# Performance work log

Hardware: AMD Instinct MI355X
Metric: run time of the kernel (lower is better)

The kernel has to match this reference:

```python
import math
import jax, jax.numpy as jnp
import numpy as np

NUM_BINS = 8
TRANS = 8
LEFT, RIGHT = -1.0, 1.0
MIN_W = MIN_H = MIN_D = 1.0e-4


def setup_inputs() -> dict:
    key = jax.random.key(0)
    ks = jax.random.split(key, 8)
    B, D, H, OUT = 524288, 16, 256, TRANS * (3 * NUM_BINS - 1)
    x = jax.random.uniform(ks[0], (B, D), jnp.float32, -0.99, 0.99)
    W0 = jax.random.normal(ks[1], (8, H), jnp.float32) * (1.0 / math.sqrt(8))
    b0 = jnp.zeros((H,), jnp.float32)
    W1 = jax.random.normal(ks[2], (H, H), jnp.float32) * (1.0 / math.sqrt(H))
    b1 = jnp.zeros((H,), jnp.float32)
    Wout = jax.random.normal(ks[3], (H, OUT), jnp.float32) * (0.1 / math.sqrt(H))
    bout = jnp.zeros((OUT,), jnp.float32)
    return {"x": x, "W0": W0, "b0": b0, "W1": W1, "b1": b1, "Wout": Wout, "bout": bout}


def _rq_spline(x, raw_w, raw_h, raw_d):
    # x: [B, T]; raw_w/raw_h: [B, T, K]; raw_d: [B, T, K-1]
    span = RIGHT - LEFT
    const = math.log(math.exp(1.0 - MIN_D) - 1.0)
    widths = jax.nn.softmax(raw_w, axis=-1)
    heights = jax.nn.softmax(raw_h, axis=-1)
    derivs = jax.nn.softplus(raw_d + const) + MIN_D
    widths = span * (MIN_W + (1.0 - MIN_W * NUM_BINS) * widths)
    heights = span * (MIN_H + (1.0 - MIN_H * NUM_BINS) * heights)
    edge_x = LEFT + jnp.pad(jnp.cumsum(widths, axis=-1), ((0, 0), (0, 0), (1, 0)))
    edge_y = LEFT + jnp.pad(jnp.cumsum(heights, axis=-1), ((0, 0), (0, 0), (1, 0)))
    derivs = jnp.pad(derivs, ((0, 0), (0, 0), (1, 1)), constant_values=1.0)
    out_mask = (x <= LEFT + 1e-3) | (x >= RIGHT - 1e-3)
    x_in = jnp.where(out_mask, 0.0, x)
    # searchsorted(right=True) - 1 == count of edges <= x_in, minus 1
    idx = jnp.clip(jnp.sum(edge_x <= x_in[..., None], axis=-1) - 1, 0, NUM_BINS - 1)
    g = lambda a: jnp.take_along_axis(a, idx[..., None], axis=-1)[..., 0]
    xk, yk = g(edge_x), g(edge_y)
    wk, hk = g(widths), g(heights)
    dk, dk1 = g(derivs), g(derivs[..., 1:])
    sk = hk / wk
    eps = (x_in - xk) / wk
    eps_term = eps * (1.0 - eps)
    eps2 = eps * eps
    beta = sk + (dk1 + dk - 2.0 * sk) * eps_term
    alpha = hk * (sk * eps2 + dk * eps_term)
    output = jnp.where(out_mask, x, yk + alpha / beta)
    logdet = (2.0 * jnp.log(sk)
              + jnp.log(dk1 * eps2 + 2.0 * sk * eps_term + dk * (1.0 - eps) ** 2)
              - 2.0 * jnp.log(beta))
    logdet = jnp.where(out_mask, 0.0, logdet)
    return output, logdet


def reference(x, W0, b0, W1, b1, Wout, bout):
    x1 = x[..., :TRANS]   # transformed half (mask == True)
    x2 = x[..., TRANS:]   # conditioning half
    h = jax.nn.relu(x2 @ W0 + b0)
    h = jax.nn.relu(h @ W1 + b1)
    raw = (h @ Wout + bout).reshape(x.shape[0], TRANS, 3 * NUM_BINS - 1)
    raw_w = raw[..., :NUM_BINS]
    raw_h = raw[..., NUM_BINS:2 * NUM_BINS]
    raw_d = raw[..., 2 * NUM_BINS:]
    y1, logdet = _rq_spline(x1, raw_w, raw_h, raw_d)
    out = jnp.concatenate([y1, x2], axis=-1)
    return out, jnp.sum(logdet, axis=-1)
```

## Files before the change

### kernel.cpp

```cpp
#include <hip/hip_runtime.h>
#include <hip/hip_bf16.h>


typedef __bf16 bf16x8 __attribute__((ext_vector_type(8)));
typedef __bf16 bf16x4v __attribute__((ext_vector_type(4)));
typedef float  f32x8 __attribute__((ext_vector_type(8)));
typedef float  f32x4 __attribute__((ext_vector_type(4)));
typedef float  f32x2 __attribute__((ext_vector_type(2)));

#define MFMA16(a,b,c) __builtin_amdgcn_mfma_f32_16x16x32_bf16((a),(b),(c),0,0,0)

#define SW_W1_OFF 8192
#define SW_WO_OFF 73728
#define SW_TOTAL  122880

#define ROWS    128
#define HSTRIDE 264
#define LOG2E   1.44269504f
#define LN2     0.69314718f
#define SPCONST 0.7806568f
#define ZSENT  (-0.00015680f)

__global__ void prep_kernel(const float* __restrict__ W0,
                            const float* __restrict__ W1,
                            const float* __restrict__ Wout,
                            const float* __restrict__ bout,
                            __bf16* __restrict__ sw)
{
  int i = blockIdx.x * 256 + threadIdx.x;
  if (i >= SW_TOTAL + 192) return;
  if (i >= SW_TOTAL){
    int np = i - SW_TOTAL;
    int t = np / 24, p = np % 24;
    float* boutp = (float*)(sw + SW_TOTAL);
    boutp[np] = (p < 23) ? bout[t*23 + p] * LOG2E : 0.f;
    return;
  }
  const float* src; int K, N, NT, li;
  bool wo = false;
  if (i < SW_W1_OFF)      { src = W0;   K = 8;   N = 256; NT = 16; li = i; }
  else if (i < SW_WO_OFF) { src = W1;   K = 256; N = 256; NT = 16; li = i - SW_W1_OFF; }
  else { src = Wout; K = 256; N = 184; NT = 12; li = i - SW_WO_OFF; wo = true; }
  int j    = li & 7;
  int l    = (li >> 3) & 63;
  int rest = li >> 9;
  int nt   = rest % NT;
  int kb   = rest / NT;
  int k = kb * 32 + ((l >> 4) << 3) + j;
  int n = nt * 16 + (l & 15);
  float v;
  if (wo){
    int t = n / 24, p = n % 24;
    v = (p < 23 && k < K) ? Wout[k*184 + t*23 + p] * LOG2E : 0.f;
  } else {
    v = (k < K && n < N) ? src[k * N + n] : 0.f;
  }
  sw[i] = (__bf16)v;
}

__device__ __forceinline__ bf16x4v relu_cvt4(f32x4 acc, float4 bb){
  f32x4 s;
  s[0] = acc[0] + bb.x; s[1] = acc[1] + bb.y;
  s[2] = acc[2] + bb.z; s[3] = acc[3] + bb.w;
  f32x4 z = {0.f, 0.f, 0.f, 0.f};
  s = __builtin_elementwise_max(s, z);
  return __builtin_convertvector(s, bf16x4v);
}

__device__ __forceinline__ bf16x4v add_cvt4(f32x4 acc, float4 bb){
  f32x4 s;
  s[0] = acc[0] + bb.x; s[1] = acc[1] + bb.y;
  s[2] = acc[2] + bb.z; s[3] = acc[3] + bb.w;
  return __builtin_convertvector(s, bf16x4v);
}

__global__ __launch_bounds__(512, 4)
void fused_kernel(const float* __restrict__ x,
                  const float* __restrict__ b0v,
                  const float* __restrict__ b1v,
                  const __bf16* __restrict__ sw,
                  float* __restrict__ out,
                  int nrows)
{
  __shared__ __align__(16) unsigned char smem[ROWS * HSTRIDE * 2];
  __bf16* hbuf = (__bf16*)smem;
  __bf16* rawb = hbuf;

  const int tid  = threadIdx.x;
  const int wave = tid >> 6;
  const int lane = tid & 63;
  const int quad = lane >> 4;
  const int l16  = lane & 15;
  const int row0 = blockIdx.x * ROWS;

  const __bf16* swW1 = sw + SW_W1_OFF;
  const __bf16* swWo = sw + SW_WO_OFF;
  const float* boutp = (const float*)(sw + SW_TOTAL);
  const f32x4 z4 = {0.f, 0.f, 0.f, 0.f};

  if (tid < 2*ROWS){
    int r = tid >> 1, hf = tid & 1;
    long g = (long)row0 + r;
    *(float4*)(out + g*16 + 8 + hf*4) = *(const float4*)(x + g*16 + 8 + hf*4);
  }

  const int mq = wave >> 1;
  const int nh = wave & 1;

  {
    bf16x8 bfr[4];
    #pragma unroll
    for (int nt = 0; nt < 4; nt++){
      bf16x8 b = {};
      if (quad == 0){
        const float* xp = x + (long)(row0 + (nh*4 + nt)*16 + l16)*16 + 8;
        float4 u = *(const float4*)xp;
        float4 v = *(const float4*)(xp + 4);
        f32x8 xf; xf[0]=u.x; xf[1]=u.y; xf[2]=u.z; xf[3]=u.w;
                  xf[4]=v.x; xf[5]=v.y; xf[6]=v.z; xf[7]=v.w;
        b = __builtin_convertvector(xf, bf16x8);
      }
      bfr[nt] = b;
    }
    #pragma unroll
    for (int mi = 0; mi < 4; mi++){
      int mt = mq*4 + mi;
      bf16x8 a = *(const bf16x8*)(sw + (mt*64 + lane)*8);
      float4 bb = *(const float4*)(b0v + mt*16 + quad*4);
      #pragma unroll
      for (int nt = 0; nt < 4; nt++){
        f32x4 acc = MFMA16(a, bfr[nt], z4);
        *(bf16x4v*)(hbuf + ((nh*4+nt)*16 + l16)*HSTRIDE + mt*16 + quad*4) = relu_cvt4(acc, bb);
      }
    }
  }
  __syncthreads();

  {
    f32x4 acc[4][4];
    #pragma unroll
    for (int mi=0;mi<4;mi++)
      #pragma unroll
      for (int bt=0;bt<4;bt++) acc[mi][bt] = z4;
    #pragma unroll
    for (int kb=0;kb<8;kb++){
      bf16x8 hf[4];
      #pragma unroll
      for (int bt=0;bt<4;bt++)
        hf[bt] = *(const bf16x8*)(hbuf + ((nh*4+bt)*16 + l16)*HSTRIDE + kb*32 + quad*8);
      #pragma unroll
      for (int mi=0;mi<4;mi++){
        bf16x8 a = *(const bf16x8*)(swW1 + ((kb*16 + mq*4 + mi)*64 + lane)*8);
        #pragma unroll
        for (int bt=0;bt<4;bt++)
          acc[mi][bt] = MFMA16(a, hf[bt], acc[mi][bt]);
      }
    }
    __syncthreads();
    #pragma unroll
    for (int mi=0;mi<4;mi++){
      int mt = mq*4 + mi;
      float4 bb = *(const float4*)(b1v + mt*16 + quad*4);
      #pragma unroll
      for (int bt=0;bt<4;bt++)
        *(bf16x4v*)(hbuf + ((nh*4+bt)*16 + l16)*HSTRIDE + mt*16 + quad*4) = relu_cvt4(acc[mi][bt], bb);
    }
  }
  __syncthreads();

  {
    const int nc = wave & 3;
    const int mh = wave >> 2;
    f32x4 acc[4][3];
    #pragma unroll
    for (int bt=0;bt<4;bt++)
      #pragma unroll
      for (int mi=0;mi<3;mi++) acc[bt][mi] = z4;
    #pragma unroll
    for (int kb=0;kb<8;kb++){
      bf16x8 hf[4];
      #pragma unroll
      for (int bt=0;bt<4;bt++)
        hf[bt] = *(const bf16x8*)(hbuf + ((mh*4+bt)*16 + l16)*HSTRIDE + kb*32 + quad*8);
      #pragma unroll
      for (int mi=0;mi<3;mi++){
        bf16x8 a = *(const bf16x8*)(swWo + ((kb*12 + nc*3 + mi)*64 + lane)*8);
        #pragma unroll
        for (int bt=0;bt<4;bt++)
          acc[bt][mi] = MFMA16(a, hf[bt], acc[bt][mi]);
      }
    }
    __syncthreads();
    #pragma unroll
    for (int mi=0;mi<3;mi++){
      int mt = nc*3 + mi;
      float4 bb = *(const float4*)(boutp + mt*16 + quad*4);
      #pragma unroll
      for (int bt=0;bt<4;bt++){
        int row = (mh*4+bt)*16 + l16;
        *(bf16x4v*)(rawb + row*HSTRIDE + mt*16 + quad*4) = add_cvt4(acc[bt][mi], bb);
      }
    }
  }
  __syncthreads();

  float ldv[2];
  #pragma unroll
  for (int pp = 0; pp < 2; pp++){
    int p   = tid + pp*512;
    int row = p >> 3;
    int t   = p & 7;
    long gr = row0 + row;
    float xv = x[gr*16 + t];

    const __bf16* rr = rawb + row*HSTRIDE + t*24;
    bf16x8 v0 = *(const bf16x8*)(rr);
    bf16x8 v1 = *(const bf16x8*)(rr + 8);
    bf16x8 v2 = *(const bf16x8*)(rr + 16);

    f32x2 ewh[8];
    f32x2 sum = {0.f, 0.f};
    #pragma unroll
    for (int i=0;i<8;i++){
      f32x2 e;
      e[0] = __builtin_amdgcn_exp2f((float)v0[i]);
      e[1] = __builtin_amdgcn_exp2f((float)v1[i]);
      ewh[i] = e; sum += e;
    }
    f32x2 scale;
    scale[0] = 1.9984f * __builtin_amdgcn_rcpf(sum[0]);
    scale[1] = 1.9984f * __builtin_amdgcn_rcpf(sum[1]);
    const f32x2 off2 = {2e-4f, 2e-4f};

    bool msk = (xv <= -0.999f) || (xv >= 0.999f);
    float xin = msk ? 0.f : xv;

    f32x2 whi = ewh[0]*scale + off2;
    f32x2 ec; ec[0] = -1.f + whi[0]; ec[1] = -1.f + whi[1];
    f32x2 xyk = {-1.f, -1.f};
    f32x2 whk = whi;
    float zk = ZSENT, zk1 = (float)v2[0];
    #pragma unroll
    for (int i=1;i<8;i++){
      whi = ewh[i]*scale + off2;
      bool le = (ec[0] <= xin);
      xyk = le ? ec : xyk;
      whk = le ? whi : whk;
      zk  = le ? (float)v2[i-1] : zk;
      zk1 = le ? ((i==7) ? ZSENT : (float)v2[i]) : zk1;
      ec += whi;
    }

    float za = zk + SPCONST, zb = zk1 + SPCONST;
    float dk  = (fmaxf(za,0.f) + __builtin_amdgcn_logf(1.f + __builtin_amdgcn_exp2f(-fabsf(za))))*LN2 + 1e-4f;
    float dk1 = (fmaxf(zb,0.f) + __builtin_amdgcn_logf(1.f + __builtin_amdgcn_exp2f(-fabsf(zb))))*LN2 + 1e-4f;

    float rwk = __builtin_amdgcn_rcpf(whk[0]);
    float sk  = whk[1] * rwk;
    float eps = (xin - xyk[0]) * rwk;
    float om  = 1.f - eps;
    float et  = eps * om;
    float e2  = eps * eps;
    float beta  = sk + (dk1 + dk - 2.f*sk) * et;
    float rb    = __builtin_amdgcn_rcpf(beta);
    float alpha = whk[1] * (sk*e2 + dk*et);
    float yv  = msk ? xv : (xyk[1] + alpha * rb);
    float num = dk1*e2 + 2.f*sk*et + dk*om*om;
    float ld  = msk ? 0.f : __builtin_amdgcn_logf(sk*sk*num*rb*rb) * LN2;

    out[gr*16 + t] = yv;
    ldv[pp] = ld;
  }

  float s0 = ldv[0], s1 = ldv[1];
  #pragma unroll
  for (int m = 1; m < 8; m <<= 1){
    s0 += __shfl_xor(s0, m);
    s1 += __shfl_xor(s1, m);
  }
  if ((lane & 7) == 0){
    int r = tid >> 3;
    out[(long)nrows*16 + row0 + r]      = s0;
    out[(long)nrows*16 + row0 + r + 64] = s1;
  }
}

extern "C" void kernel_launch(void* const* d_in, const int* in_sizes, int n_in,
                              void* d_out, int out_size, void* d_ws, size_t ws_size,
                              hipStream_t stream)
{
  const float* x    = (const float*)d_in[0];
  const float* W0   = (const float*)d_in[1];
  const float* b0   = (const float*)d_in[2];
  const float* W1   = (const float*)d_in[3];
  const float* b1   = (const float*)d_in[4];
  const float* Wout = (const float*)d_in[5];
  const float* bout = (const float*)d_in[6];
  float* out = (float*)d_out;
  __bf16* sw = (__bf16*)d_ws;

  int nrows = in_sizes[0] / 16;
  int ntiles = nrows / ROWS;

  prep_kernel<<<(SW_TOTAL + 192 + 255)/256, 256, 0, stream>>>(W0, W1, Wout, bout, sw);
  fused_kernel<<<ntiles, 512, 0, stream>>>(x, b0, b1, sw, out, nrows);
}
```

Measured before the change: 219.3 us.

## Switch first two MLP layers to 32x32x16 MFMA with bias-initialized accumulators

Moves the first two GEMM layers from 16x16x32 to 32x32x16 bf16 MFMA tiles. The prep kernel's weight swizzle is rewritten to match, and the W0 block shrinks because K=8 now only needs one 16-deep slice. Biases are loaded straight into the accumulators, which removes the per-element bias adds in the epilogues of all three layers. Larger tiles cut the LDS fragment loads per FLOP, but raise accumulator register pressure and change the LDS access patterns.

```diff
diff --git a/kernel.cpp b/kernel.cpp
--- a/kernel.cpp
+++ b/kernel.cpp
@@ -4,15 +4,17 @@
 
 typedef __bf16 bf16x8 __attribute__((ext_vector_type(8)));
 typedef __bf16 bf16x4v __attribute__((ext_vector_type(4)));
+typedef float  f32x16 __attribute__((ext_vector_type(16)));
 typedef float  f32x8 __attribute__((ext_vector_type(8)));
 typedef float  f32x4 __attribute__((ext_vector_type(4)));
 typedef float  f32x2 __attribute__((ext_vector_type(2)));
 
 #define MFMA16(a,b,c) __builtin_amdgcn_mfma_f32_16x16x32_bf16((a),(b),(c),0,0,0)
-
-#define SW_W1_OFF 8192
-#define SW_WO_OFF 73728
-#define SW_TOTAL  122880
+#define MFMA32(a,b,c) __builtin_amdgcn_mfma_f32_32x32x16_bf16((a),(b),(c),0,0,0)
+
+#define SW_W1_OFF 4096
+#define SW_WO_OFF 69632
+#define SW_TOTAL  118784
 
 #define ROWS    128
 #define HSTRIDE 264
@@ -36,41 +38,37 @@
     boutp[np] = (p < 23) ? bout[t*23 + p] * LOG2E : 0.f;
     return;
   }
-  const float* src; int K, N, NT, li;
-  bool wo = false;
-  if (i < SW_W1_OFF)      { src = W0;   K = 8;   N = 256; NT = 16; li = i; }
-  else if (i < SW_WO_OFF) { src = W1;   K = 256; N = 256; NT = 16; li = i - SW_W1_OFF; }
-  else { src = Wout; K = 256; N = 184; NT = 12; li = i - SW_WO_OFF; wo = true; }
-  int j    = li & 7;
-  int l    = (li >> 3) & 63;
-  int rest = li >> 9;
-  int nt   = rest % NT;
-  int kb   = rest / NT;
-  int k = kb * 32 + ((l >> 4) << 3) + j;
-  int n = nt * 16 + (l & 15);
-  float v;
-  if (wo){
+  if (i < SW_WO_OFF){
+    const float* src; int K; int li;
+    if (i < SW_W1_OFF){ src = W0; K = 8;   li = i; }
+    else              { src = W1; K = 256; li = i - SW_W1_OFF; }
+    int j    = li & 7;
+    int l    = (li >> 3) & 63;
+    int rest = li >> 9;
+    int mt   = rest & 7;
+    int ks   = rest >> 3;
+    int k = ks*16 + ((l >> 5) << 3) + j;
+    int n = mt*32 + (l & 31);
+    sw[i] = (__bf16)((k < K) ? src[k*256 + n] : 0.f);
+  } else {
+    int li   = i - SW_WO_OFF;
+    int j    = li & 7;
+    int l    = (li >> 3) & 63;
+    int rest = li >> 9;
+    int nt   = rest % 12;
+    int kb   = rest / 12;
+    int k = kb*32 + ((l >> 4) << 3) + j;
+    int n = nt*16 + (l & 15);
     int t = n / 24, p = n % 24;
-    v = (p < 23 && k < K) ? Wout[k*184 + t*23 + p] * LOG2E : 0.f;
-  } else {
-    v = (k < K && n < N) ? src[k * N + n] : 0.f;
-  }
-  sw[i] = (__bf16)v;
+    sw[i] = (__bf16)((p < 23) ? Wout[k*184 + t*23 + p] * LOG2E : 0.f);
+  }
 }
 
-__device__ __forceinline__ bf16x4v relu_cvt4(f32x4 acc, float4 bb){
+__device__ __forceinline__ bf16x4v reluq(const f32x16& c, int Q){
   f32x4 s;
-  s[0] = acc[0] + bb.x; s[1] = acc[1] + bb.y;
-  s[2] = acc[2] + bb.z; s[3] = acc[3] + bb.w;
-  f32x4 z = {0.f, 0.f, 0.f, 0.f};
+  s[0] = c[4*Q+0]; s[1] = c[4*Q+1]; s[2] = c[4*Q+2]; s[3] = c[4*Q+3];
+  const f32x4 z = {0.f, 0.f, 0.f, 0.f};
   s = __builtin_elementwise_max(s, z);
-  return __builtin_convertvector(s, bf16x4v);
-}
-
-__device__ __forceinline__ bf16x4v add_cvt4(f32x4 acc, float4 bb){
-  f32x4 s;
-  s[0] = acc[0] + bb.x; s[1] = acc[1] + bb.y;
-  s[2] = acc[2] + bb.z; s[3] = acc[3] + bb.w;
   return __builtin_convertvector(s, bf16x4v);
 }
 
@@ -91,12 +89,13 @@
   const int lane = tid & 63;
   const int quad = lane >> 4;
   const int l16  = lane & 15;
+  const int l32  = lane & 31;
+  const int hi   = lane >> 5;
   const int row0 = blockIdx.x * ROWS;
 
   const __bf16* swW1 = sw + SW_W1_OFF;
   const __bf16* swWo = sw + SW_WO_OFF;
   const float* boutp = (const float*)(sw + SW_TOTAL);
-  const f32x4 z4 = {0.f, 0.f, 0.f, 0.f};
 
   if (tid < 2*ROWS){
     int r = tid >> 1, hf = tid & 1;
@@ -104,67 +103,77 @@
     *(float4*)(out + g*16 + 8 + hf*4) = *(const float4*)(x + g*16 + 8 + hf*4);
   }
 
-  const int mq = wave >> 1;
-  const int nh = wave & 1;
-
   {
     bf16x8 bfr[4];
     #pragma unroll
-    for (int nt = 0; nt < 4; nt++){
+    for (int bt = 0; bt < 4; bt++){
       bf16x8 b = {};
-      if (quad == 0){
-        const float* xp = x + (long)(row0 + (nh*4 + nt)*16 + l16)*16 + 8;
+      if (hi == 0){
+        const float* xp = x + (long)(row0 + bt*32 + l32)*16 + 8;
         float4 u = *(const float4*)xp;
         float4 v = *(const float4*)(xp + 4);
         f32x8 xf; xf[0]=u.x; xf[1]=u.y; xf[2]=u.z; xf[3]=u.w;
                   xf[4]=v.x; xf[5]=v.y; xf[6]=v.z; xf[7]=v.w;
         b = __builtin_convertvector(xf, bf16x8);
       }
-      bfr[nt] = b;
-    }
-    #pragma unroll
-    for (int mi = 0; mi < 4; mi++){
-      int mt = mq*4 + mi;
-      bf16x8 a = *(const bf16x8*)(sw + (mt*64 + lane)*8);
-      float4 bb = *(const float4*)(b0v + mt*16 + quad*4);
-      #pragma unroll
-      for (int nt = 0; nt < 4; nt++){
-        f32x4 acc = MFMA16(a, bfr[nt], z4);
-        *(bf16x4v*)(hbuf + ((nh*4+nt)*16 + l16)*HSTRIDE + mt*16 + quad*4) = relu_cvt4(acc, bb);
-      }
+      bfr[bt] = b;
+    }
+    bf16x8 a = *(const bf16x8*)(sw + (wave*64 + lane)*8);
+    f32x16 ci;
+    #pragma unroll
+    for (int Q = 0; Q < 4; Q++){
+      float4 bq = *(const float4*)(b0v + wave*32 + Q*8 + hi*4);
+      ci[4*Q+0]=bq.x; ci[4*Q+1]=bq.y; ci[4*Q+2]=bq.z; ci[4*Q+3]=bq.w;
+    }
+    #pragma unroll
+    for (int bt = 0; bt < 4; bt++){
+      f32x16 c = MFMA32(a, bfr[bt], ci);
+      __bf16* hp = hbuf + (bt*32 + l32)*HSTRIDE + wave*32 + hi*4;
+      #pragma unroll
+      for (int Q = 0; Q < 4; Q++)
+        *(bf16x4v*)(hp + Q*8) = reluq(c, Q);
     }
   }
   __syncthreads();
 
   {
-    f32x4 acc[4][4];
-    #pragma unroll
-    for (int mi=0;mi<4;mi++)
-      #pragma unroll
-      for (int bt=0;bt<4;bt++) acc[mi][bt] = z4;
-    #pragma unroll
-    for (int kb=0;kb<8;kb++){
-      bf16x8 hf[4];
-      #pragma unroll
-      for (int bt=0;bt<4;bt++)
-        hf[bt] = *(const bf16x8*)(hbuf + ((nh*4+bt)*16 + l16)*HSTRIDE + kb*32 + quad*8);
-      #pragma unroll
-      for (int mi=0;mi<4;mi++){
-        bf16x8 a = *(const bf16x8*)(swW1 + ((kb*16 + mq*4 + mi)*64 + lane)*8);
+    const int mp = wave >> 1;
+    const int bh = wave & 1;
+    f32x16 acc[2][2];
+    #pragma unroll
+    for (int mi = 0; mi < 2; mi++){
+      f32x16 c;
+      #pragma unroll
+      for (int Q = 0; Q < 4; Q++){
+        float4 bq = *(const float4*)(b1v + (mp*2+mi)*32 + Q*8 + hi*4);
+        c[4*Q+0]=bq.x; c[4*Q+1]=bq.y; c[4*Q+2]=bq.z; c[4*Q+3]=bq.w;
+      }
+      acc[mi][0] = c; acc[mi][1] = c;
+    }
+    #pragma unroll
+    for (int ks = 0; ks < 16; ks++){
+      bf16x8 hf[2];
+      #pragma unroll
+      for (int bi = 0; bi < 2; bi++)
+        hf[bi] = *(const bf16x8*)(hbuf + ((bh*2+bi)*32 + l32)*HSTRIDE + ks*16 + hi*8);
+      #pragma unroll
+      for (int mi = 0; mi < 2; mi++){
+        bf16x8 a = *(const bf16x8*)(swW1 + ((ks*8 + mp*2 + mi)*64 + lane)*8);
         #pragma unroll
-        for (int bt=0;bt<4;bt++)
-          acc[mi][bt] = MFMA16(a, hf[bt], acc[mi][bt]);
+        for (int bi = 0; bi < 2; bi++)
+          acc[mi][bi] = MFMA32(a, hf[bi], acc[mi][bi]);
       }
     }
     __syncthreads();
     #pragma unroll
-    for (int mi=0;mi<4;mi++){
-      int mt = mq*4 + mi;
-      float4 bb = *(const float4*)(b1v + mt*16 + quad*4);
-      #pragma unroll
-      for (int bt=0;bt<4;bt++)
-        *(bf16x4v*)(hbuf + ((nh*4+bt)*16 + l16)*HSTRIDE + mt*16 + quad*4) = relu_cvt4(acc[mi][bt], bb);
-    }
+    for (int mi = 0; mi < 2; mi++)
+      #pragma unroll
+      for (int bi = 0; bi < 2; bi++){
+        __bf16* hp = hbuf + ((bh*2+bi)*32 + l32)*HSTRIDE + (mp*2+mi)*32 + hi*4;
+        #pragma unroll
+        for (int Q = 0; Q < 4; Q++)
+          *(bf16x4v*)(hp + Q*8) = reluq(acc[mi][bi], Q);
+      }
   }
   __syncthreads();
 
@@ -173,32 +182,35 @@
     const int mh = wave >> 2;
     f32x4 acc[4][3];
     #pragma unroll
-    for (int bt=0;bt<4;bt++)
-      #pragma unroll
-      for (int mi=0;mi<3;mi++) acc[bt][mi] = z4;
-    #pragma unroll
-    for (int kb=0;kb<8;kb++){
+    for (int mi = 0; mi < 3; mi++){
+      float4 bb = *(const float4*)(boutp + (nc*3+mi)*16 + quad*4);
+      f32x4 c; c[0]=bb.x; c[1]=bb.y; c[2]=bb.z; c[3]=bb.w;
+      #pragma unroll
+      for (int bt = 0; bt < 4; bt++) acc[bt][mi] = c;
+    }
+    #pragma unroll
+    for (int kb = 0; kb < 8; kb++){
       bf16x8 hf[4];
       #pragma unroll
-      for (int bt=0;bt<4;bt++)
+      for (int bt = 0; bt < 4; bt++)
         hf[bt] = *(const bf16x8*)(hbuf + ((mh*4+bt)*16 + l16)*HSTRIDE + kb*32 + quad*8);
       #pragma unroll
-      for (int mi=0;mi<3;mi++){
+      for (int mi = 0; mi < 3; mi++){
         bf16x8 a = *(const bf16x8*)(swWo + ((kb*12 + nc*3 + mi)*64 + lane)*8);
         #pragma unroll
-        for (int bt=0;bt<4;bt++)
+        for (int bt = 0; bt < 4; bt++)
           acc[bt][mi] = MFMA16(a, hf[bt], acc[bt][mi]);
       }
     }
     __syncthreads();
     #pragma unroll
-    for (int mi=0;mi<3;mi++){
+    for (int mi = 0; mi < 3; mi++){
       int mt = nc*3 + mi;
-      float4 bb = *(const float4*)(boutp + mt*16 + quad*4);
-      #pragma unroll
-      for (int bt=0;bt<4;bt++){
+      #pragma unroll
+      for (int bt = 0; bt < 4; bt++){
         int row = (mh*4+bt)*16 + l16;
-        *(bf16x4v*)(rawb + row*HSTRIDE + mt*16 + quad*4) = add_cvt4(acc[bt][mi], bb);
+        *(bf16x4v*)(rawb + row*HSTRIDE + mt*16 + quad*4) =
+            __builtin_convertvector(acc[bt][mi], bf16x4v);
       }
     }
   }
```

Result: slower. 228.6 us (+4.2%).

## Halve rows per block, redistribute MFMA tiles, and fold bias into accumulator init

Applied to the files above, without the earlier changes.

Each block now handles 64 rows instead of 128 and launch bounds ask for 8 blocks per CU instead of 4. The layer-2 work split changes from 4x4 tiles per wave to 2 weight tiles by 4 row tiles, and the output layer uses 2 row tiles per wave. Biases are loaded as the initial MFMA accumulator instead of being added afterwards. The aim is higher occupancy from less LDS and fewer registers per block, at the cost of loading each weight fragment for fewer rows, so weight traffic per row doubles.

```diff
diff --git a/kernel.cpp b/kernel.cpp
--- a/kernel.cpp
+++ b/kernel.cpp
@@ -14,7 +14,7 @@
 #define SW_WO_OFF 73728
 #define SW_TOTAL  122880
 
-#define ROWS    128
+#define ROWS    64
 #define HSTRIDE 264
 #define LOG2E   1.44269504f
 #define LN2     0.69314718f
@@ -58,23 +58,19 @@
   sw[i] = (__bf16)v;
 }
 
-__device__ __forceinline__ bf16x4v relu_cvt4(f32x4 acc, float4 bb){
-  f32x4 s;
-  s[0] = acc[0] + bb.x; s[1] = acc[1] + bb.y;
-  s[2] = acc[2] + bb.z; s[3] = acc[3] + bb.w;
-  f32x4 z = {0.f, 0.f, 0.f, 0.f};
+__device__ __forceinline__ bf16x4v relu_cvt(f32x4 s){
+  const f32x4 z = {0.f, 0.f, 0.f, 0.f};
   s = __builtin_elementwise_max(s, z);
   return __builtin_convertvector(s, bf16x4v);
 }
 
-__device__ __forceinline__ bf16x4v add_cvt4(f32x4 acc, float4 bb){
-  f32x4 s;
-  s[0] = acc[0] + bb.x; s[1] = acc[1] + bb.y;
-  s[2] = acc[2] + bb.z; s[3] = acc[3] + bb.w;
-  return __builtin_convertvector(s, bf16x4v);
-}
-
-__global__ __launch_bounds__(512, 4)
+__device__ __forceinline__ f32x4 bias4(const float* p){
+  float4 bb = *(const float4*)p;
+  f32x4 c; c[0]=bb.x; c[1]=bb.y; c[2]=bb.z; c[3]=bb.w;
+  return c;
+}
+
+__global__ __launch_bounds__(512, 8)
 void fused_kernel(const float* __restrict__ x,
                   const float* __restrict__ b0v,
                   const float* __restrict__ b1v,
@@ -96,7 +92,6 @@
   const __bf16* swW1 = sw + SW_W1_OFF;
   const __bf16* swWo = sw + SW_WO_OFF;
   const float* boutp = (const float*)(sw + SW_TOTAL);
-  const f32x4 z4 = {0.f, 0.f, 0.f, 0.f};
 
   if (tid < 2*ROWS){
     int r = tid >> 1, hf = tid & 1;
@@ -104,16 +99,15 @@
     *(float4*)(out + g*16 + 8 + hf*4) = *(const float4*)(x + g*16 + 8 + hf*4);
   }
 
-  const int mq = wave >> 1;
-  const int nh = wave & 1;
-
-  {
-    bf16x8 bfr[4];
-    #pragma unroll
-    for (int nt = 0; nt < 4; nt++){
+  {
+    const int mq = wave >> 1;
+    const int nh = wave & 1;
+    bf16x8 bfr[2];
+    #pragma unroll
+    for (int nt = 0; nt < 2; nt++){
       bf16x8 b = {};
       if (quad == 0){
-        const float* xp = x + (long)(row0 + (nh*4 + nt)*16 + l16)*16 + 8;
+        const float* xp = x + (long)(row0 + nh*32 + nt*16 + l16)*16 + 8;
         float4 u = *(const float4*)xp;
         float4 v = *(const float4*)(xp + 4);
         f32x8 xf; xf[0]=u.x; xf[1]=u.y; xf[2]=u.z; xf[3]=u.w;
@@ -126,90 +120,90 @@
     for (int mi = 0; mi < 4; mi++){
       int mt = mq*4 + mi;
       bf16x8 a = *(const bf16x8*)(sw + (mt*64 + lane)*8);
-      float4 bb = *(const float4*)(b0v + mt*16 + quad*4);
-      #pragma unroll
-      for (int nt = 0; nt < 4; nt++){
-        f32x4 acc = MFMA16(a, bfr[nt], z4);
-        *(bf16x4v*)(hbuf + ((nh*4+nt)*16 + l16)*HSTRIDE + mt*16 + quad*4) = relu_cvt4(acc, bb);
+      f32x4 ci = bias4(b0v + mt*16 + quad*4);
+      #pragma unroll
+      for (int nt = 0; nt < 2; nt++){
+        f32x4 acc = MFMA16(a, bfr[nt], ci);
+        *(bf16x4v*)(hbuf + (nh*32 + nt*16 + l16)*HSTRIDE + mt*16 + quad*4) = relu_cvt(acc);
       }
     }
   }
   __syncthreads();
 
   {
-    f32x4 acc[4][4];
-    #pragma unroll
-    for (int mi=0;mi<4;mi++)
-      #pragma unroll
-      for (int bt=0;bt<4;bt++) acc[mi][bt] = z4;
-    #pragma unroll
-    for (int kb=0;kb<8;kb++){
+    f32x4 acc[2][4];
+    #pragma unroll
+    for (int mi = 0; mi < 2; mi++){
+      f32x4 ci = bias4(b1v + (wave*2 + mi)*16 + quad*4);
+      #pragma unroll
+      for (int bt = 0; bt < 4; bt++) acc[mi][bt] = ci;
+    }
+    #pragma unroll
+    for (int kb = 0; kb < 8; kb++){
       bf16x8 hf[4];
       #pragma unroll
-      for (int bt=0;bt<4;bt++)
-        hf[bt] = *(const bf16x8*)(hbuf + ((nh*4+bt)*16 + l16)*HSTRIDE + kb*32 + quad*8);
-      #pragma unroll
-      for (int mi=0;mi<4;mi++){
-        bf16x8 a = *(const bf16x8*)(swW1 + ((kb*16 + mq*4 + mi)*64 + lane)*8);
+      for (int bt = 0; bt < 4; bt++)
+        hf[bt] = *(const bf16x8*)(hbuf + (bt*16 + l16)*HSTRIDE + kb*32 + quad*8);
+      #pragma unroll
+      for (int mi = 0; mi < 2; mi++){
+        bf16x8 a = *(const bf16x8*)(swW1 + ((kb*16 + wave*2 + mi)*64 + lane)*8);
         #pragma unroll
-        for (int bt=0;bt<4;bt++)
+        for (int bt = 0; bt < 4; bt++)
           acc[mi][bt] = MFMA16(a, hf[bt], acc[mi][bt]);
       }
     }
     __syncthreads();
     #pragma unroll
-    for (int mi=0;mi<4;mi++){
-      int mt = mq*4 + mi;
-      float4 bb = *(const float4*)(b1v + mt*16 + quad*4);
-      #pragma unroll
-      for (int bt=0;bt<4;bt++)
-        *(bf16x4v*)(hbuf + ((nh*4+bt)*16 + l16)*HSTRIDE + mt*16 + quad*4) = relu_cvt4(acc[mi][bt], bb);
-    }
+    for (int mi = 0; mi < 2; mi++)
+      #pragma unroll
+      for (int bt = 0; bt < 4; bt++)
+        *(bf16x4v*)(hbuf + (bt*16 + l16)*HSTRIDE + (wave*2+mi)*16 + quad*4) =
+            relu_cvt(acc[mi][bt]);
   }
   __syncthreads();
 
   {
     const int nc = wave & 3;
     const int mh = wave >> 2;
-    f32x4 acc[4][3];
-    #pragma unroll
-    for (int bt=0;bt<4;bt++)
-      #pragma unroll
-      for (int mi=0;mi<3;mi++) acc[bt][mi] = z4;
-    #pragma unroll
-    for (int kb=0;kb<8;kb++){
-      bf16x8 hf[4];
-      #pragma unroll
-      for (int bt=0;bt<4;bt++)
-        hf[bt] = *(const bf16x8*)(hbuf + ((mh*4+bt)*16 + l16)*HSTRIDE + kb*32 + quad*8);
-      #pragma unroll
-      for (int mi=0;mi<3;mi++){
+    f32x4 acc[2][3];
+    #pragma unroll
+    for (int mi = 0; mi < 3; mi++){
+      f32x4 ci = bias4(boutp + (nc*3+mi)*16 + quad*4);
+      #pragma unroll
+      for (int bt = 0; bt < 2; bt++) acc[bt][mi] = ci;
+    }
+    #pragma unroll
+    for (int kb = 0; kb < 8; kb++){
+      bf16x8 hf[2];
+      #pragma unroll
+      for (int bt = 0; bt < 2; bt++)
+        hf[bt] = *(const bf16x8*)(hbuf + ((mh*2+bt)*16 + l16)*HSTRIDE + kb*32 + quad*8);
+      #pragma unroll
+      for (int mi = 0; mi < 3; mi++){
         bf16x8 a = *(const bf16x8*)(swWo + ((kb*12 + nc*3 + mi)*64 + lane)*8);
         #pragma unroll
-        for (int bt=0;bt<4;bt++)
+        for (int bt = 0; bt < 2; bt++)
           acc[bt][mi] = MFMA16(a, hf[bt], acc[bt][mi]);
       }
     }
     __syncthreads();
     #pragma unroll
-    for (int mi=0;mi<3;mi++){
+    for (int mi = 0; mi < 3; mi++){
       int mt = nc*3 + mi;
-      float4 bb = *(const float4*)(boutp + mt*16 + quad*4);
-      #pragma unroll
-      for (int bt=0;bt<4;bt++){
-        int row = (mh*4+bt)*16 + l16;
-        *(bf16x4v*)(rawb + row*HSTRIDE + mt*16 + quad*4) = add_cvt4(acc[bt][mi], bb);
+      #pragma unroll
+      for (int bt = 0; bt < 2; bt++){
+        int row = (mh*2+bt)*16 + l16;
+        *(bf16x4v*)(rawb + row*HSTRIDE + mt*16 + quad*4) =
+            __builtin_convertvector(acc[bt][mi], bf16x4v);
       }
     }
   }
   __syncthreads();
 
-  float ldv[2];
-  #pragma unroll
-  for (int pp = 0; pp < 2; pp++){
-    int p   = tid + pp*512;
-    int row = p >> 3;
-    int t   = p & 7;
+  float ld;
+  {
+    int row = tid >> 3;
+    int t   = tid & 7;
     long gr = row0 + row;
     float xv = x[gr*16 + t];
 
@@ -266,23 +260,18 @@
     float alpha = whk[1] * (sk*e2 + dk*et);
     float yv  = msk ? xv : (xyk[1] + alpha * rb);
     float num = dk1*e2 + 2.f*sk*et + dk*om*om;
-    float ld  = msk ? 0.f : __builtin_amdgcn_logf(sk*sk*num*rb*rb) * LN2;
+    float ldv = msk ? 0.f : __builtin_amdgcn_logf(sk*sk*num*rb*rb) * LN2;
 
     out[gr*16 + t] = yv;
-    ldv[pp] = ld;
-  }
-
-  float s0 = ldv[0], s1 = ldv[1];
+    ld = ldv;
+  }
+
+  float s0 = ld;
   #pragma unroll
-  for (int m = 1; m < 8; m <<= 1){
+  for (int m = 1; m < 8; m <<= 1)
     s0 += __shfl_xor(s0, m);
-    s1 += __shfl_xor(s1, m);
-  }
-  if ((lane & 7) == 0){
-    int r = tid >> 3;
-    out[(long)nrows*16 + row0 + r]      = s0;
-    out[(long)nrows*16 + row0 + r + 64] = s1;
-  }
+  if ((lane & 7) == 0)
+    out[(long)nrows*16 + row0 + (tid >> 3)] = s0;
 }
 
 extern "C" void kernel_launch(void* const* d_in, const int* in_sizes, int n_in,
```

Result: slower. 241.7 us (+10.2%).

## Retile wave work split in hidden and output GEMMs, fold bias into MFMA accumulator

Applied to the files above, without the earlier changes.

Each wave now covers 8 (or 6) weight M-tiles across 2 batch tiles instead of 4x4 (or 3x4), so fewer LDS activation fragments are read per k-step while more weight fragments come from global memory. Biases are loaded into the initial accumulators rather than added after the MFMA, which removes the per-element bias adds. The change trades LDS traffic for more global/L2 weight loads per wave and shifts register usage.

```diff
diff --git a/kernel.cpp b/kernel.cpp
--- a/kernel.cpp
+++ b/kernel.cpp
@@ -58,20 +58,16 @@
   sw[i] = (__bf16)v;
 }
 
-__device__ __forceinline__ bf16x4v relu_cvt4(f32x4 acc, float4 bb){
-  f32x4 s;
-  s[0] = acc[0] + bb.x; s[1] = acc[1] + bb.y;
-  s[2] = acc[2] + bb.z; s[3] = acc[3] + bb.w;
-  f32x4 z = {0.f, 0.f, 0.f, 0.f};
+__device__ __forceinline__ bf16x4v relu_cvt(f32x4 s){
+  const f32x4 z = {0.f, 0.f, 0.f, 0.f};
   s = __builtin_elementwise_max(s, z);
   return __builtin_convertvector(s, bf16x4v);
 }
 
-__device__ __forceinline__ bf16x4v add_cvt4(f32x4 acc, float4 bb){
-  f32x4 s;
-  s[0] = acc[0] + bb.x; s[1] = acc[1] + bb.y;
-  s[2] = acc[2] + bb.z; s[3] = acc[3] + bb.w;
-  return __builtin_convertvector(s, bf16x4v);
+__device__ __forceinline__ f32x4 bias4(const float* p){
+  float4 bb = *(const float4*)p;
+  f32x4 c; c[0]=bb.x; c[1]=bb.y; c[2]=bb.z; c[3]=bb.w;
+  return c;
 }
 
 __global__ __launch_bounds__(512, 4)
@@ -96,7 +92,6 @@
   const __bf16* swW1 = sw + SW_W1_OFF;
   const __bf16* swWo = sw + SW_WO_OFF;
   const float* boutp = (const float*)(sw + SW_TOTAL);
-  const f32x4 z4 = {0.f, 0.f, 0.f, 0.f};
 
   if (tid < 2*ROWS){
     int r = tid >> 1, hf = tid & 1;
@@ -126,79 +121,79 @@
     for (int mi = 0; mi < 4; mi++){
       int mt = mq*4 + mi;
       bf16x8 a = *(const bf16x8*)(sw + (mt*64 + lane)*8);
-      float4 bb = *(const float4*)(b0v + mt*16 + quad*4);
+      f32x4 ci = bias4(b0v + mt*16 + quad*4);
       #pragma unroll
       for (int nt = 0; nt < 4; nt++){
-        f32x4 acc = MFMA16(a, bfr[nt], z4);
-        *(bf16x4v*)(hbuf + ((nh*4+nt)*16 + l16)*HSTRIDE + mt*16 + quad*4) = relu_cvt4(acc, bb);
+        f32x4 acc = MFMA16(a, bfr[nt], ci);
+        *(bf16x4v*)(hbuf + ((nh*4+nt)*16 + l16)*HSTRIDE + mt*16 + quad*4) = relu_cvt(acc);
       }
     }
   }
   __syncthreads();
 
   {
-    f32x4 acc[4][4];
-    #pragma unroll
-    for (int mi=0;mi<4;mi++)
-      #pragma unroll
-      for (int bt=0;bt<4;bt++) acc[mi][bt] = z4;
-    #pragma unroll
-    for (int kb=0;kb<8;kb++){
-      bf16x8 hf[4];
-      #pragma unroll
-      for (int bt=0;bt<4;bt++)
-        hf[bt] = *(const bf16x8*)(hbuf + ((nh*4+bt)*16 + l16)*HSTRIDE + kb*32 + quad*8);
-      #pragma unroll
-      for (int mi=0;mi<4;mi++){
-        bf16x8 a = *(const bf16x8*)(swW1 + ((kb*16 + mq*4 + mi)*64 + lane)*8);
-        #pragma unroll
-        for (int bt=0;bt<4;bt++)
-          acc[mi][bt] = MFMA16(a, hf[bt], acc[mi][bt]);
+    const int mg = wave >> 2;
+    const int bg = wave & 3;
+    f32x4 acc[8][2];
+    #pragma unroll
+    for (int mi = 0; mi < 8; mi++){
+      f32x4 ci = bias4(b1v + (mg*8 + mi)*16 + quad*4);
+      acc[mi][0] = ci; acc[mi][1] = ci;
+    }
+    #pragma unroll
+    for (int kb = 0; kb < 8; kb++){
+      bf16x8 hf[2];
+      #pragma unroll
+      for (int bi = 0; bi < 2; bi++)
+        hf[bi] = *(const bf16x8*)(hbuf + ((bg*2+bi)*16 + l16)*HSTRIDE + kb*32 + quad*8);
+      #pragma unroll
+      for (int mi = 0; mi < 8; mi++){
+        bf16x8 a = *(const bf16x8*)(swW1 + ((kb*16 + mg*8 + mi)*64 + lane)*8);
+        acc[mi][0] = MFMA16(a, hf[0], acc[mi][0]);
+        acc[mi][1] = MFMA16(a, hf[1], acc[mi][1]);
       }
     }
     __syncthreads();
     #pragma unroll
-    for (int mi=0;mi<4;mi++){
-      int mt = mq*4 + mi;
-      float4 bb = *(const float4*)(b1v + mt*16 + quad*4);
-      #pragma unroll
-      for (int bt=0;bt<4;bt++)
-        *(bf16x4v*)(hbuf + ((nh*4+bt)*16 + l16)*HSTRIDE + mt*16 + quad*4) = relu_cvt4(acc[mi][bt], bb);
-    }
+    for (int mi = 0; mi < 8; mi++)
+      #pragma unroll
+      for (int bi = 0; bi < 2; bi++)
+        *(bf16x4v*)(hbuf + ((bg*2+bi)*16 + l16)*HSTRIDE + (mg*8+mi)*16 + quad*4) =
+            relu_cvt(acc[mi][bi]);
   }
   __syncthreads();
 
   {
-    const int nc = wave & 3;
-    const int mh = wave >> 2;
-    f32x4 acc[4][3];
-    #pragma unroll
-    for (int bt=0;bt<4;bt++)
-      #pragma unroll
-      for (int mi=0;mi<3;mi++) acc[bt][mi] = z4;
-    #pragma unroll
-    for (int kb=0;kb<8;kb++){
-      bf16x8 hf[4];
-      #pragma unroll
-      for (int bt=0;bt<4;bt++)
-        hf[bt] = *(const bf16x8*)(hbuf + ((mh*4+bt)*16 + l16)*HSTRIDE + kb*32 + quad*8);
-      #pragma unroll
-      for (int mi=0;mi<3;mi++){
-        bf16x8 a = *(const bf16x8*)(swWo + ((kb*12 + nc*3 + mi)*64 + lane)*8);
-        #pragma unroll
-        for (int bt=0;bt<4;bt++)
-          acc[bt][mi] = MFMA16(a, hf[bt], acc[bt][mi]);
+    const int ng = wave >> 2;
+    const int bg = wave & 3;
+    f32x4 acc[6][2];
+    #pragma unroll
+    for (int mi = 0; mi < 6; mi++){
+      f32x4 ci = bias4(boutp + (ng*6+mi)*16 + quad*4);
+      acc[mi][0] = ci; acc[mi][1] = ci;
+    }
+    #pragma unroll
+    for (int kb = 0; kb < 8; kb++){
+      bf16x8 hf[2];
+      #pragma unroll
+      for (int bi = 0; bi < 2; bi++)
+        hf[bi] = *(const bf16x8*)(hbuf + ((bg*2+bi)*16 + l16)*HSTRIDE + kb*32 + quad*8);
+      #pragma unroll
+      for (int mi = 0; mi < 6; mi++){
+        bf16x8 a = *(const bf16x8*)(swWo + ((kb*12 + ng*6 + mi)*64 + lane)*8);
+        acc[mi][0] = MFMA16(a, hf[0], acc[mi][0]);
+        acc[mi][1] = MFMA16(a, hf[1], acc[mi][1]);
       }
     }
     __syncthreads();
     #pragma unroll
-    for (int mi=0;mi<3;mi++){
-      int mt = nc*3 + mi;
-      float4 bb = *(const float4*)(boutp + mt*16 + quad*4);
-      #pragma unroll
-      for (int bt=0;bt<4;bt++){
-        int row = (mh*4+bt)*16 + l16;
-        *(bf16x4v*)(rawb + row*HSTRIDE + mt*16 + quad*4) = add_cvt4(acc[bt][mi], bb);
+    for (int mi = 0; mi < 6; mi++){
+      int mt = ng*6 + mi;
+      #pragma unroll
+      for (int bi = 0; bi < 2; bi++){
+        int row = (bg*2+bi)*16 + l16;
+        *(bf16x4v*)(rawb + row*HSTRIDE + mt*16 + quad*4) =
+            __builtin_convertvector(acc[mi][bi], bf16x4v);
       }
     }
   }
@@ -290,8 +285,8 @@
                               hipStream_t stream)
 {
   const float* x    = (const float*)d_in[0];
+  const float* b0   = (const float*)d_in[2];
   const float* W0   = (const float*)d_in[1];
-  const float* b0   = (const float*)d_in[2];
   const float* W1   = (const float*)d_in[3];
   const float* b1   = (const float*)d_in[4];
   const float* Wout = (const float*)d_in[5];
```

New measurement: 242.3 us. +10.5%, slower.
